# Kernel tuning notes

Measured on AMD Instinct MI355X. Metric: run time of the kernel, lower is better.

## Reference

```python
import jax, jax.numpy as jnp
import numpy as np

NGRAM = 2
NUM_HEADS = 16
NUM_BUCKETS = 32
EMBED_DIM = 1024
REAL_T = 512
BSZ = 4


def setup_inputs() -> dict:
    key = jax.random.key(0)
    ks = jax.random.split(key, 10)
    tgt_len = (1 + NGRAM) * REAL_T
    E, H, NB = EMBED_DIM, NUM_HEADS, NUM_BUCKETS
    w = 0.02
    return {
        "query": jax.random.normal(ks[0], (tgt_len, BSZ, E), jnp.float32),
        "self_attn_mask": jnp.zeros((REAL_T, REAL_T), jnp.float32),
        "ngram_mask_matrix": jnp.zeros((NGRAM, REAL_T, 2 * REAL_T), jnp.float32),
        "i_buckets_main_stream": jax.random.randint(ks[1], (BSZ, REAL_T, REAL_T), 0, NB, jnp.int32),
        "i_bucket_relative_stream": jax.random.randint(ks[2], (BSZ, REAL_T, 2 * REAL_T), 0, NB, jnp.int32),
        "in_proj_weight": jax.random.normal(ks[3], (3 * E, E), jnp.float32) * w,
        "in_proj_bias": jnp.zeros((3 * E,), jnp.float32),
        "out_proj_weight": jax.random.normal(ks[4], (E, E), jnp.float32) * w,
        "out_proj_bias": jnp.zeros((E,), jnp.float32),
        "relative_weight": jax.random.normal(ks[5], (NB * H, E), jnp.float32) * w,
        "relative_bias": jnp.zeros((NB * H,), jnp.float32),
    }


def _forward(query, self_attn_mask, ngram_mask_matrix,
             ib_main, ib_rel,
             in_proj_weight, in_proj_bias, out_proj_weight, out_proj_bias,
             relative_weight, relative_bias):
    tgt_len, bsz, E = query.shape
    H, n = NUM_HEADS, NGRAM
    hd = E // H
    nb = relative_weight.shape[0] // H
    T = tgt_len // (1 + n)
    scaling = hd ** -0.5

    # fused qkv projection
    qkv = query @ in_proj_weight.T + in_proj_bias  # [tgt, B, 3E]
    q, k, v = jnp.split(qkv, 3, axis=-1)
    q = q * scaling

    def to_bh(x):  # [tgt, B, E] -> [B*H, tgt, hd]
        return x.reshape(tgt_len, bsz * H, hd).transpose(1, 0, 2)
    q, k, v = to_bh(q), to_bh(k), to_bh(v)

    h_main = query[:T]                                  # [T, B, E]
    h_pred = query[T:].reshape(n, T, bsz, E)            # [n, T, B, E]
    q_main, k_main, v_main = q[:, :T], k[:, :T], v[:, :T]            # [BH, T, hd]
    def pred(x):  # [BH, n*T, hd] -> [n, BH, T, hd]
        return x[:, T:].reshape(bsz * H, n, T, hd).transpose(1, 0, 2, 3)
    q_pred, k_pred, v_pred = pred(q), pred(k), pred(v)

    # ---- main stream ----
    aw_main = jnp.einsum('bth,bsh->bts', q_main, k_main)  # [BH, T, T]
    # relative bias: per-token bucket values gathered by bucket index
    vals_main = h_main.transpose(1, 0, 2) @ relative_weight.T + relative_bias  # [B, T, nb*H]
    vals_main = vals_main.reshape(bsz, T, nb, H).transpose(0, 3, 1, 2)         # [B, H, T, nb]
    ib = jnp.broadcast_to(ib_main[:, None].astype(jnp.int32), (bsz, H, T, T))
    rel_main = jnp.take_along_axis(vals_main, ib, axis=-1).reshape(bsz * H, T, T)
    aw_main = aw_main + rel_main + self_attn_mask[None]
    p_main = jax.nn.softmax(aw_main, axis=-1)
    attn_main = jnp.einsum('bts,bsh->bth', p_main, v_main)  # [BH, T, hd]
    attn_main = attn_main.transpose(1, 0, 2).reshape(T, bsz, E)

    # ---- ngram predict streams ----
    k_ng = jnp.concatenate([jnp.broadcast_to(k_main[None], (n,) + k_main.shape), k_pred], axis=2)  # [n, BH, 2T, hd]
    v_ng = jnp.concatenate([jnp.broadcast_to(v_main[None], (n,) + v_main.shape), v_pred], axis=2)
    aw_ng = jnp.einsum('nbtc,nbsc->nbts', q_pred, k_ng)  # [n, BH, T, 2T]

    vals_ng = h_pred.transpose(0, 2, 1, 3) @ relative_weight.T + relative_bias  # [n, B, T, nb*H]
    vals_ng = vals_ng.reshape(n, bsz, T, nb, H).transpose(0, 1, 4, 2, 3)        # [n, B, H, T, nb]
    ibr = jnp.broadcast_to(ib_rel[None, :, None].astype(jnp.int32), (n, bsz, H, T, 2 * T))
    rel_ng = jnp.take_along_axis(vals_ng, ibr, axis=-1).reshape(n, bsz * H, T, 2 * T)
    aw_ng = aw_ng + rel_ng + ngram_mask_matrix[:, None]
    p_ng = jax.nn.softmax(aw_ng, axis=-1)
    attn_ng = jnp.einsum('nbts,nbsc->nbtc', p_ng, v_ng)  # [n, BH, T, hd]
    attn_ng = attn_ng.transpose(0, 2, 1, 3).reshape(n * T, bsz, E)

    attn = jnp.concatenate([attn_main, attn_ng], axis=0)  # [tgt, B, E]
    return attn @ out_proj_weight.T + out_proj_bias


def reference(query, self_attn_mask, ngram_mask_matrix,
              i_buckets_main_stream, i_bucket_relative_stream,
              in_proj_weight, in_proj_bias, out_proj_weight, out_proj_bias,
              relative_weight, relative_bias):
    return _forward(query, self_attn_mask, ngram_mask_matrix,
                    i_buckets_main_stream, i_bucket_relative_stream,
                    in_proj_weight, in_proj_bias, out_proj_weight, out_proj_bias,
                    relative_weight, relative_bias)
```

## Files before the change

kernel.cpp:

```cpp
#include <hip/hip_runtime.h>

#define TSEQ 512
#define BSZN 4
#define NH 16
#define NBN 32
#define EMB 1024
#define HD 64
#define TGT 1536
#define MROWS 6144
#define LOG2E 1.44269504088896f

typedef unsigned short ushort_t;
typedef __bf16 bf8 __attribute__((ext_vector_type(8)));
typedef __bf16 bf2_t __attribute__((ext_vector_type(2)));
typedef ushort_t u16x8v __attribute__((ext_vector_type(8)));
typedef float f32x4 __attribute__((ext_vector_type(4)));

__device__ __forceinline__ unsigned short f2bf(float f) {
  return __builtin_bit_cast(unsigned short, (__bf16)f);
}

__device__ __forceinline__ float bf2f(unsigned short u) {
  return __builtin_bit_cast(float, (unsigned int)u << 16);
}

__device__ __forceinline__ unsigned int packbf(float a, float b) {
  bf2_t t;
  t[0] = (__bf16)a;
  t[1] = (__bf16)b;
  return __builtin_bit_cast(unsigned int, t);
}

__device__ __forceinline__ void gload16(const void* g, void* l) {
  __builtin_amdgcn_global_load_lds(
      (const __attribute__((address_space(1))) void*)g,
      (__attribute__((address_space(3))) void*)l, 16, 0, 0);
}

__device__ __forceinline__ f32x4 mfma_bf16(bf8 a, bf8 b, f32x4 c) {
  return __builtin_amdgcn_mfma_f32_16x16x32_bf16(a, b, c, 0, 0, 0);
}

__device__ __forceinline__ float lanebcast(float v, int srclane) {
  return __builtin_bit_cast(float,
      __builtin_amdgcn_ds_bpermute(srclane * 4, __builtin_bit_cast(int, v)));
}

__global__ void prep_all_kernel(const float* __restrict__ q, const float* __restrict__ win,
                                const float* __restrict__ wout, const float* __restrict__ wrel,
                                const int* __restrict__ ibm, const int* __restrict__ ibr,
                                const float* __restrict__ mm, const float* __restrict__ mng,
                                ushort_t* __restrict__ qo, ushort_t* __restrict__ wino,
                                ushort_t* __restrict__ wouto, ushort_t* __restrict__ wrelo,
                                unsigned int* __restrict__ cm, unsigned int* __restrict__ cng) {
  const int i = blockIdx.x * blockDim.x + threadIdx.x;
  const int n0 = 1572864, n1 = 786432, n2 = 262144, n3 = 131072;
  const int ncvt = n0 + n1 + n2 + n3;
  const int nm = 262144, nr = 1048576;
  if (i < ncvt) {
    const float* src;
    ushort_t* dst;
    int off;
    if (i < n0) { src = q; dst = qo; off = i; }
    else if (i < n0 + n1) { src = win; dst = wino; off = i - n0; }
    else if (i < n0 + n1 + n2) { src = wout; dst = wouto; off = i - n0 - n1; }
    else { src = wrel; dst = wrelo; off = i - n0 - n1 - n2; }
    const float4 v = reinterpret_cast<const float4*>(src)[off];
    ushort4 o;
    o.x = f2bf(v.x); o.y = f2bf(v.y); o.z = f2bf(v.z); o.w = f2bf(v.w);
    reinterpret_cast<ushort4*>(dst)[off] = o;
  } else if (i < ncvt + nm) {
    const int f = (i - ncvt) * 4;
    const int4 ib = *reinterpret_cast<const int4*>(ibm + f);
    const float4 mk = *reinterpret_cast<const float4*>(mm + (f & 262143));
    uint4 o;
    o.x = ((unsigned int)f2bf(mk.x * LOG2E) << 16) | ((unsigned int)ib.x & 31u);
    o.y = ((unsigned int)f2bf(mk.y * LOG2E) << 16) | ((unsigned int)ib.y & 31u);
    o.z = ((unsigned int)f2bf(mk.z * LOG2E) << 16) | ((unsigned int)ib.z & 31u);
    o.w = ((unsigned int)f2bf(mk.w * LOG2E) << 16) | ((unsigned int)ib.w & 31u);
    *reinterpret_cast<uint4*>(cm + f) = o;
  } else if (i < ncvt + nm + nr) {
    const int f = (i - ncvt - nm) * 4;
    const int ib_off = ((f >> 20) << 19) + (f & 524287);
    const int mk_off = f & 1048575;
    const int4 ib = *reinterpret_cast<const int4*>(ibr + ib_off);
    const float4 mk = *reinterpret_cast<const float4*>(mng + mk_off);
    uint4 o;
    o.x = ((unsigned int)f2bf(mk.x * LOG2E) << 16) | ((unsigned int)ib.x & 31u);
    o.y = ((unsigned int)f2bf(mk.y * LOG2E) << 16) | ((unsigned int)ib.y & 31u);
    o.z = ((unsigned int)f2bf(mk.z * LOG2E) << 16) | ((unsigned int)ib.z & 31u);
    o.w = ((unsigned int)f2bf(mk.w * LOG2E) << 16) | ((unsigned int)ib.w & 31u);
    *reinterpret_cast<uint4*>(cng + f) = o;
  }
}

template <int MODE>
__global__ __launch_bounds__(256) void gemm_bt(
    const ushort_t* __restrict__ A, const ushort_t* __restrict__ B,
    const float* __restrict__ bias, float* __restrict__ Cf,
    ushort_t* __restrict__ Qo, ushort_t* __restrict__ Ko, ushort_t* __restrict__ Vto,
    int M, int N, int K) {
  __shared__ ushort_t lds[16384];
  ushort_t* lA = lds;
  ushort_t* lB = lds + 8192;

  const int tid = threadIdx.x;
  const int lane = tid & 63;
  const int wid = tid >> 6;
  const int l15 = lane & 15, l4 = lane >> 4;
  const int bm = blockIdx.y, bn = blockIdx.x;
  const int wm = (wid >> 1) * 64, wn = (wid & 1) * 64;

  f32x4 acc[4][4] = {};

  const int r8 = tid >> 3;
  const int c8 = ((tid & 7) ^ (r8 & 7)) * 8;
  const ushort_t* Ag = A + (size_t)(bm * 128 + r8) * K + c8;
  const ushort_t* Bg = B + (size_t)(bn * 128 + r8) * K + c8;
  ushort_t* lAp = lA + tid * 8;
  ushort_t* lBp = lB + tid * 8;

  for (int kt = 0; kt < K; kt += 64) {
    __syncthreads();
#pragma unroll
    for (int i = 0; i < 4; ++i) {
      gload16(Ag + (size_t)i * 32 * K + kt, lAp + i * 2048);
      gload16(Bg + (size_t)i * 32 * K + kt, lBp + i * 2048);
    }
    __syncthreads();
#pragma unroll
    for (int k0 = 0; k0 < 2; ++k0) {
      bf8 af[4], bv[4];
#pragma unroll
      for (int mi = 0; mi < 4; ++mi) {
        const int row = wm + mi * 16 + l15;
        const int slot = (k0 * 4 + l4) ^ (row & 7);
        af[mi] = *reinterpret_cast<const bf8*>(lA + row * 64 + slot * 8);
      }
#pragma unroll
      for (int ni = 0; ni < 4; ++ni) {
        const int row = wn + ni * 16 + l15;
        const int slot = (k0 * 4 + l4) ^ (row & 7);
        bv[ni] = *reinterpret_cast<const bf8*>(lB + row * 64 + slot * 8);
      }
#pragma unroll
      for (int mi = 0; mi < 4; ++mi)
#pragma unroll
        for (int ni = 0; ni < 4; ++ni)
          acc[mi][ni] = mfma_bf16(af[mi], bv[ni], acc[mi][ni]);
    }
  }

  if (MODE == 0 && bn >= 16) {
    __syncthreads();
    char* tb = reinterpret_cast<char*>(lds);
#pragma unroll
    for (int ni = 0; ni < 4; ++ni) {
      const int colloc = wn + ni * 16 + l15;
      const float bc = bias[bn * 128 + colloc];
      const unsigned int swz = (colloc & 7) << 4;
#pragma unroll
      for (int mi = 0; mi < 4; ++mi) {
        const int t_loc = (wm >> 2) + mi * 4 + l4;
        f32x4 v = acc[mi][ni];
#pragma unroll
        for (int r = 0; r < 4; ++r) {
          const int byteoff = colloc * 256 + ((r * 64 + t_loc * 2) ^ swz);
          *reinterpret_cast<ushort_t*>(tb + byteoff) = f2bf(v[r] + bc);
        }
      }
    }
    __syncthreads();
    const int tglob0 = bm * 32;
#pragma unroll
    for (int p = 0; p < 2; ++p) {
      const int pair = wid * 2 + p;
      const int bb = pair >> 1;
      const int hl = pair & 1;
      const int hh = (bn - 16) * 2 + hl;
      const int bh = bb * NH + hh;
      const int tch = lane & 3;
#pragma unroll
      for (int ii = 0; ii < 4; ++ii) {
        const int dloc = ii * 16 + (lane >> 2);
        const int colloc = hl * 64 + dloc;
        const int byteoff = colloc * 256 + ((bb * 64 + tch * 16) ^ ((colloc & 7) << 4));
        const u16x8v val = *reinterpret_cast<const u16x8v*>(tb + byteoff);
        *reinterpret_cast<u16x8v*>(
            Vto + ((size_t)bh * HD + dloc) * TGT + tglob0 + tch * 8) = val;
      }
    }
    return;
  }

#pragma unroll
  for (int ni = 0; ni < 4; ++ni) {
    const int col = bn * 128 + wn + ni * 16 + l15;
    const float bc = bias[col];
#pragma unroll
    for (int mi = 0; mi < 4; ++mi) {
      const int row0 = bm * 128 + wm + mi * 16 + l4 * 4;
      f32x4 v = acc[mi][ni];
#pragma unroll
      for (int r = 0; r < 4; ++r) {
        const int row = row0 + r;
        float val = v[r] + bc;
        if (MODE == 0) {
          const int part = col >> 10;
          const int cc = col & 1023;
          const int h = cc >> 6, d = cc & 63;
          const int t = row >> 2, bb = row & 3;
          const int bh = bb * NH + h;
          if (part == 0) {
            Qo[((size_t)bh * TGT + t) * HD + d] = f2bf(val * (0.125f * LOG2E));
          } else {
            Ko[((size_t)bh * TGT + t) * HD + d] = f2bf(val);
          }
        } else if (MODE == 3) {
          const int hh = col & 15, nb = col >> 4;
          const int qg = row >> 2, bb2 = row & 3;
          Qo[(((size_t)(bb2 * NH + hh)) * TGT + qg) * NBN + nb] = f2bf(val * LOG2E);
        } else {
          Cf[(size_t)row * N + col] = val;
        }
      }
    }
  }
}

__global__ __launch_bounds__(256, 3) void attn_kernel(
    const ushort_t* __restrict__ Q, const ushort_t* __restrict__ Kb,
    const ushort_t* __restrict__ Vt, const ushort_t* __restrict__ VMh,
    const unsigned int* __restrict__ comb_main, const unsigned int* __restrict__ comb_ng,
    ushort_t* __restrict__ AT) {
  __shared__ unsigned char kbuf[2][8192];
  __shared__ unsigned char vbuf[2][8192];
  __shared__ ushort_t vmt16[4][1088];
  __shared__ unsigned int pbl[4][576];

  const int tid = threadIdx.x;
  const int lane = tid & 63, wid = tid >> 6;
  const int l15 = lane & 15, l4 = lane >> 4;

  const int n = blockIdx.x;
  const int xcd = n & 7;
  const int b = xcd >> 1;
  const int idx = (xcd & 1) * 96 + (n >> 3);
  const int h = idx / 12;
  const int rem = idx - h * 12;
  const int z = rem >> 2;
  const int blk = rem & 3;
  const int g = (z == 0) ? 0 : z - 1;
  const int bh = b * NH + h;
  const int t0 = blk * 128 + wid * 32;
  const int qrow0 = (z == 0) ? t0 : TSEQ + g * TSEQ + t0;
  const int nsb = (z == 0) ? 8 : 16;

  {
    const ushort_t* src = VMh + ((size_t)bh * TGT + qrow0) * NBN;
    ushort_t* dst = vmt16[wid];
#pragma unroll
    for (int half = 0; half < 2; ++half) {
      const u16x8v v = *reinterpret_cast<const u16x8v*>(src + half * 512 + lane * 8);
      const int r = half * 16 + (lane >> 2);
      const int c0 = (lane & 3) * 8;
#pragma unroll
      for (int i = 0; i < 8; ++i) dst[r * 34 + c0 + i] = v[i];
    }
  }

  bf8 qf[2][2];
#pragma unroll
  for (int th = 0; th < 2; ++th)
#pragma unroll
    for (int hf = 0; hf < 2; ++hf)
      qf[th][hf] = *reinterpret_cast<const bf8*>(
          &Q[((size_t)bh * TGT + qrow0 + th * 16 + l15) * HD + hf * 32 + l4 * 8]);

  const unsigned int* cb[2];
  {
    const unsigned int* cbase = (z == 0)
        ? comb_main + (size_t)b * TSEQ * TSEQ
        : comb_ng + (size_t)(b * 2 + g) * TSEQ * (2 * TSEQ);
    const int sstr = (z == 0) ? TSEQ : 2 * TSEQ;
    cb[0] = cbase + (size_t)(t0 + l15) * sstr;
    cb[1] = cbase + (size_t)(t0 + 16 + l15) * sstr;
  }

  float m_run[2] = {-1e30f, -1e30f};
  float l_run[2] = {0.f, 0.f};
  f32x4 oacc[2][4] = {};

  const int r8 = lane >> 3;
  const int swzs = ((lane & 7) ^ r8) << 4;
  const int swzr = (l15 & 7) << 4;

  auto stage = [&](int sb, int bf) {
    const int srow0 = (sb < 8) ? sb * 64 : TSEQ + g * TSEQ + (sb - 8) * 64;
    const ushort_t* ks = Kb + ((size_t)bh * TGT + srow0 + wid * 16 + r8) * HD + (swzs >> 1);
    gload16(ks, &kbuf[bf][wid * 2048 + lane * 16]);
    gload16(ks + 8 * HD, &kbuf[bf][wid * 2048 + 1024 + lane * 16]);
    const ushort_t* vs = Vt + ((size_t)bh * HD + wid * 16 + r8) * TGT + srow0 + (swzs >> 1);
    gload16(vs, &vbuf[bf][wid * 2048 + lane * 16]);
    gload16(vs + 8 * TGT, &vbuf[bf][wid * 2048 + 1024 + lane * 16]);
  };

  stage(0, 0);
  asm volatile("s_waitcnt vmcnt(0)" ::: "memory");
  __builtin_amdgcn_s_barrier();

  int cur = 0;
  for (int sb = 0; sb < nsb; ++sb) {
    const int scol = sb * 64;
    if (sb + 1 < nsb) stage(sb + 1, cur ^ 1);

    const unsigned char* kb = kbuf[cur];
    const unsigned char* vbb = vbuf[cur];

    bf8 kf[4][2];
#pragma unroll
    for (int j = 0; j < 4; ++j) {
      const int row = j * 16 + l15;
      kf[j][0] = *reinterpret_cast<const bf8*>(kb + row * 128 + ((l4 * 16) ^ swzr));
      kf[j][1] = *reinterpret_cast<const bf8*>(kb + row * 128 + ((64 + l4 * 16) ^ swzr));
    }

#pragma unroll
    for (int th = 0; th < 2; ++th) {
      const unsigned int* cwp = cb[th] + scol + l4 * 4;
      const uint4 c0 = *reinterpret_cast<const uint4*>(cwp);
      const uint4 c1 = *reinterpret_cast<const uint4*>(cwp + 16);
      const uint4 c2 = *reinterpret_cast<const uint4*>(cwp + 32);
      const uint4 c3 = *reinterpret_cast<const uint4*>(cwp + 48);
      const unsigned int cwa[4][4] = {{c0.x, c0.y, c0.z, c0.w},
                                      {c1.x, c1.y, c1.z, c1.w},
                                      {c2.x, c2.y, c2.z, c2.w},
                                      {c3.x, c3.y, c3.z, c3.w}};
      f32x4 st[4];
#pragma unroll
      for (int j = 0; j < 4; ++j) {
        f32x4 s4 = {};
        s4 = mfma_bf16(kf[j][0], qf[th][0], s4);
        s4 = mfma_bf16(kf[j][1], qf[th][1], s4);
        st[j] = s4;
      }
      const ushort_t* vrow = vmt16[wid] + (th * 16 + l15) * 34;
      float vals[4][4];
      float mx = -1e30f;
#pragma unroll
      for (int j = 0; j < 4; ++j) {
#pragma unroll
        for (int r = 0; r < 4; ++r) {
          const unsigned int w = cwa[j][r];
          const float v = st[j][r] + __builtin_bit_cast(float, w & 0xffff0000u) +
                          bf2f(vrow[w & 31u]);
          vals[j][r] = v;
          mx = fmaxf(mx, v);
        }
      }
      mx = fmaxf(mx, __shfl_xor(mx, 16));
      mx = fmaxf(mx, __shfl_xor(mx, 32));

      const float oldm = m_run[th];
      if (!__all(mx - oldm <= 8.f)) {
        const float newm = fmaxf(oldm, mx);
        const float fct = (oldm <= -1e30f) ? 0.f : exp2f(oldm - newm);
        f32x4 rs;
        rs[0] = lanebcast(fct, l4 * 4 + 0);
        rs[1] = lanebcast(fct, l4 * 4 + 1);
        rs[2] = lanebcast(fct, l4 * 4 + 2);
        rs[3] = lanebcast(fct, l4 * 4 + 3);
#pragma unroll
        for (int dt = 0; dt < 4; ++dt) oacc[th][dt] *= rs;
        l_run[th] *= fct;
        m_run[th] = newm;
      }
      const float mref = m_run[th];

      unsigned int pk[4][2];
      float lsum = 0.f;
#pragma unroll
      for (int j = 0; j < 4; ++j) {
        const float p0 = exp2f(vals[j][0] - mref);
        const float p1 = exp2f(vals[j][1] - mref);
        const float p2 = exp2f(vals[j][2] - mref);
        const float p3 = exp2f(vals[j][3] - mref);
        lsum += (p0 + p1) + (p2 + p3);
        pk[j][0] = packbf(p0, p1);
        pk[j][1] = packbf(p2, p3);
      }
      lsum += __shfl_xor(lsum, 16);
      lsum += __shfl_xor(lsum, 32);
      l_run[th] += lsum;

      {
        unsigned int* prow = &pbl[wid][l15 * 36];
#pragma unroll
        for (int j = 0; j < 4; ++j) {
          uint2 w2;
          w2.x = pk[j][0];
          w2.y = pk[j][1];
          *reinterpret_cast<uint2*>(&prow[j * 8 + l4 * 2]) = w2;
        }
      }
      const unsigned char* pbase = reinterpret_cast<const unsigned char*>(&pbl[wid][0]);
#pragma unroll
      for (int k32 = 0; k32 < 2; ++k32) {
        const bf8 pa = *reinterpret_cast<const bf8*>(
            pbase + l15 * 144 + k32 * 64 + l4 * 16);
#pragma unroll
        for (int dt = 0; dt < 4; ++dt) {
          const bf8 vb = *reinterpret_cast<const bf8*>(
              vbb + (dt * 16 + l15) * 128 + ((k32 * 64 + l4 * 16) ^ swzr));
          oacc[th][dt] = mfma_bf16(pa, vb, oacc[th][dt]);
        }
      }
    }

    asm volatile("s_waitcnt vmcnt(0)" ::: "memory");
    __builtin_amdgcn_s_barrier();
    cur ^= 1;
  }

#pragma unroll
  for (int th = 0; th < 2; ++th) {
    const float linv = 1.f / l_run[th];
    f32x4 bs;
    bs[0] = lanebcast(linv, l4 * 4 + 0);
    bs[1] = lanebcast(linv, l4 * 4 + 1);
    bs[2] = lanebcast(linv, l4 * 4 + 2);
    bs[3] = lanebcast(linv, l4 * 4 + 3);
#pragma unroll
    for (int dt = 0; dt < 4; ++dt) {
#pragma unroll
      for (int r = 0; r < 4; ++r) {
        const int tout = qrow0 + th * 16 + l4 * 4 + r;
        AT[((size_t)tout * BSZN + b) * EMB + h * HD + dt * 16 + l15] =
            f2bf(oacc[th][dt][r] * bs[r]);
      }
    }
  }
}

extern "C" void kernel_launch(void* const* d_in, const int* in_sizes, int n_in,
                              void* d_out, int out_size, void* d_ws, size_t ws_size,
                              hipStream_t stream) {
  const float* query     = (const float*)d_in[0];
  const float* mask_main = (const float*)d_in[1];
  const float* mask_ng   = (const float*)d_in[2];
  const int*   ib_main   = (const int*)d_in[3];
  const int*   ib_rel    = (const int*)d_in[4];
  const float* w_in      = (const float*)d_in[5];
  const float* b_in      = (const float*)d_in[6];
  const float* w_out     = (const float*)d_in[7];
  const float* b_out     = (const float*)d_in[8];
  const float* w_rel     = (const float*)d_in[9];
  const float* b_rel     = (const float*)d_in[10];
  float* out = (float*)d_out;

  ushort_t* qbf    = (ushort_t*)d_ws;
  ushort_t* winbf  = qbf + 6291456;
  ushort_t* woutbf = winbf + 3145728;
  ushort_t* relwbf = woutbf + 1048576;
  ushort_t* Qb     = relwbf + 524288;
  ushort_t* Kbuf   = Qb + 6291456;
  ushort_t* Vtb    = Kbuf + 6291456;
  ushort_t* VMh    = Vtb + 6291456;
  unsigned int* comb_main = (unsigned int*)(VMh + 3145728);
  unsigned int* comb_ng   = comb_main + 1048576;
  ushort_t* AT     = qbf;

  {
    const int total = 2752512 + 262144 + 1048576;
    prep_all_kernel<<<(total + 255) / 256, 256, 0, stream>>>(
        query, w_in, w_out, w_rel, ib_main, ib_rel, mask_main, mask_ng,
        qbf, winbf, woutbf, relwbf, comb_main, comb_ng);
  }

  gemm_bt<0><<<dim3(24, 48), 256, 0, stream>>>(qbf, winbf, b_in, nullptr,
                                               Qb, Kbuf, Vtb, MROWS, 3072, 1024);
  gemm_bt<3><<<dim3(4, 48), 256, 0, stream>>>(qbf, relwbf, b_rel, nullptr,
                                              VMh, nullptr, nullptr, MROWS, 512, 1024);
  attn_kernel<<<768, 256, 0, stream>>>(Qb, Kbuf, Vtb, VMh, comb_main, comb_ng, AT);
  gemm_bt<2><<<dim3(8, 48), 256, 0, stream>>>(AT, woutbf, b_out, out,
                                              nullptr, nullptr, nullptr, MROWS, 1024, 1024);
}
```

Measured before the change: 212.8 us.

## Fuse relative-bucket GEMM into QKV GEMM launch and add MFMA priority hints

Merges the relative-position projection GEMM into the QKV projection launch by adding four extra column-blocks that read the relative weights and write the bucket-value tensor. This removes one kernel launch and its tail, and fills the grid more evenly. It also wraps MFMA sequences in s_setprio in both the GEMM and attention kernels, and hoists the comb-word loads and both S MFMA tiles ahead of the softmax in the attention loop. The hoisting raises register pressure in the attention kernel, which is launched with an occupancy bound of 3.

```diff
diff --git a/kernel.cpp b/kernel.cpp
--- a/kernel.cpp
+++ b/kernel.cpp
@@ -99,7 +99,8 @@
     const ushort_t* __restrict__ A, const ushort_t* __restrict__ B,
     const float* __restrict__ bias, float* __restrict__ Cf,
     ushort_t* __restrict__ Qo, ushort_t* __restrict__ Ko, ushort_t* __restrict__ Vto,
-    int M, int N, int K) {
+    const ushort_t* __restrict__ B2, const float* __restrict__ bias2,
+    ushort_t* __restrict__ VMo, int M, int N, int K) {
   __shared__ ushort_t lds[16384];
   ushort_t* lA = lds;
   ushort_t* lB = lds + 8192;
@@ -110,13 +111,15 @@
   const int l15 = lane & 15, l4 = lane >> 4;
   const int bm = blockIdx.y, bn = blockIdx.x;
   const int wm = (wid >> 1) * 64, wn = (wid & 1) * 64;
+  const bool isrel = (MODE == 0) && (bn >= 24);
 
   f32x4 acc[4][4] = {};
 
   const int r8 = tid >> 3;
   const int c8 = ((tid & 7) ^ (r8 & 7)) * 8;
   const ushort_t* Ag = A + (size_t)(bm * 128 + r8) * K + c8;
-  const ushort_t* Bg = B + (size_t)(bn * 128 + r8) * K + c8;
+  const ushort_t* Bg = isrel ? B2 + (size_t)((bn - 24) * 128 + r8) * K + c8
+                             : B + (size_t)(bn * 128 + r8) * K + c8;
   ushort_t* lAp = lA + tid * 8;
   ushort_t* lBp = lB + tid * 8;
 
@@ -143,15 +146,17 @@
         const int slot = (k0 * 4 + l4) ^ (row & 7);
         bv[ni] = *reinterpret_cast<const bf8*>(lB + row * 64 + slot * 8);
       }
+      __builtin_amdgcn_s_setprio(1);
 #pragma unroll
       for (int mi = 0; mi < 4; ++mi)
 #pragma unroll
         for (int ni = 0; ni < 4; ++ni)
           acc[mi][ni] = mfma_bf16(af[mi], bv[ni], acc[mi][ni]);
-    }
-  }
-
-  if (MODE == 0 && bn >= 16) {
+      __builtin_amdgcn_s_setprio(0);
+    }
+  }
+
+  if (MODE == 0 && bn >= 16 && bn < 24) {
     __syncthreads();
     char* tb = reinterpret_cast<char*>(lds);
 #pragma unroll
@@ -195,8 +200,10 @@
 
 #pragma unroll
   for (int ni = 0; ni < 4; ++ni) {
-    const int col = bn * 128 + wn + ni * 16 + l15;
-    const float bc = bias[col];
+    const int colloc = wn + ni * 16 + l15;
+    const int col = bn * 128 + colloc;
+    const int colrel = (bn - 24) * 128 + colloc;
+    const float bc = isrel ? bias2[colrel] : bias[col];
 #pragma unroll
     for (int mi = 0; mi < 4; ++mi) {
       const int row0 = bm * 128 + wm + mi * 16 + l4 * 4;
@@ -206,20 +213,21 @@
         const int row = row0 + r;
         float val = v[r] + bc;
         if (MODE == 0) {
-          const int part = col >> 10;
-          const int cc = col & 1023;
-          const int h = cc >> 6, d = cc & 63;
-          const int t = row >> 2, bb = row & 3;
-          const int bh = bb * NH + h;
-          if (part == 0) {
-            Qo[((size_t)bh * TGT + t) * HD + d] = f2bf(val * (0.125f * LOG2E));
+          if (isrel) {
+            const int hh = colrel & 15, nb = colrel >> 4;
+            const int qg = row >> 2, bb2 = row & 3;
+            VMo[(((size_t)(bb2 * NH + hh)) * TGT + qg) * NBN + nb] = f2bf(val * LOG2E);
           } else {
-            Ko[((size_t)bh * TGT + t) * HD + d] = f2bf(val);
+            const int cc = col & 1023;
+            const int h = cc >> 6, d = cc & 63;
+            const int t = row >> 2, bb = row & 3;
+            const int bh = bb * NH + h;
+            if (col < 1024) {
+              Qo[((size_t)bh * TGT + t) * HD + d] = f2bf(val * (0.125f * LOG2E));
+            } else {
+              Ko[((size_t)bh * TGT + t) * HD + d] = f2bf(val);
+            }
           }
-        } else if (MODE == 3) {
-          const int hh = col & 15, nb = col >> 4;
-          const int qg = row >> 2, bb2 = row & 3;
-          Qo[(((size_t)(bb2 * NH + hh)) * TGT + qg) * NBN + nb] = f2bf(val * LOG2E);
         } else {
           Cf[(size_t)row * N + col] = val;
         }
@@ -317,6 +325,16 @@
     const unsigned char* kb = kbuf[cur];
     const unsigned char* vbb = vbuf[cur];
 
+    uint4 cw[2][4];
+#pragma unroll
+    for (int th = 0; th < 2; ++th) {
+      const unsigned int* cwp = cb[th] + scol + l4 * 4;
+      cw[th][0] = *reinterpret_cast<const uint4*>(cwp);
+      cw[th][1] = *reinterpret_cast<const uint4*>(cwp + 16);
+      cw[th][2] = *reinterpret_cast<const uint4*>(cwp + 32);
+      cw[th][3] = *reinterpret_cast<const uint4*>(cwp + 48);
+    }
+
     bf8 kf[4][2];
 #pragma unroll
     for (int j = 0; j < 4; ++j) {
@@ -324,39 +342,33 @@
       kf[j][0] = *reinterpret_cast<const bf8*>(kb + row * 128 + ((l4 * 16) ^ swzr));
       kf[j][1] = *reinterpret_cast<const bf8*>(kb + row * 128 + ((64 + l4 * 16) ^ swzr));
     }
-
-#pragma unroll
-    for (int th = 0; th < 2; ++th) {
-      const unsigned int* cwp = cb[th] + scol + l4 * 4;
-      const uint4 c0 = *reinterpret_cast<const uint4*>(cwp);
-      const uint4 c1 = *reinterpret_cast<const uint4*>(cwp + 16);
-      const uint4 c2 = *reinterpret_cast<const uint4*>(cwp + 32);
-      const uint4 c3 = *reinterpret_cast<const uint4*>(cwp + 48);
-      const unsigned int cwa[4][4] = {{c0.x, c0.y, c0.z, c0.w},
-                                      {c1.x, c1.y, c1.z, c1.w},
-                                      {c2.x, c2.y, c2.z, c2.w},
-                                      {c3.x, c3.y, c3.z, c3.w}};
-      f32x4 st[4];
+    f32x4 st[2][4];
+    __builtin_amdgcn_s_setprio(1);
+#pragma unroll
+    for (int th = 0; th < 2; ++th)
 #pragma unroll
       for (int j = 0; j < 4; ++j) {
         f32x4 s4 = {};
         s4 = mfma_bf16(kf[j][0], qf[th][0], s4);
         s4 = mfma_bf16(kf[j][1], qf[th][1], s4);
-        st[j] = s4;
-      }
+        st[th][j] = s4;
+      }
+    __builtin_amdgcn_s_setprio(0);
+
+#pragma unroll
+    for (int th = 0; th < 2; ++th) {
       const ushort_t* vrow = vmt16[wid] + (th * 16 + l15) * 34;
       float vals[4][4];
       float mx = -1e30f;
 #pragma unroll
       for (int j = 0; j < 4; ++j) {
-#pragma unroll
-        for (int r = 0; r < 4; ++r) {
-          const unsigned int w = cwa[j][r];
-          const float v = st[j][r] + __builtin_bit_cast(float, w & 0xffff0000u) +
-                          bf2f(vrow[w & 31u]);
-          vals[j][r] = v;
-          mx = fmaxf(mx, v);
-        }
+        const unsigned int w0 = cw[th][j].x, w1 = cw[th][j].y;
+        const unsigned int w2 = cw[th][j].z, w3 = cw[th][j].w;
+        vals[j][0] = st[th][j][0] + __builtin_bit_cast(float, w0 & 0xffff0000u) + bf2f(vrow[w0 & 31u]);
+        vals[j][1] = st[th][j][1] + __builtin_bit_cast(float, w1 & 0xffff0000u) + bf2f(vrow[w1 & 31u]);
+        vals[j][2] = st[th][j][2] + __builtin_bit_cast(float, w2 & 0xffff0000u) + bf2f(vrow[w2 & 31u]);
+        vals[j][3] = st[th][j][3] + __builtin_bit_cast(float, w3 & 0xffff0000u) + bf2f(vrow[w3 & 31u]);
+        mx = fmaxf(mx, fmaxf(fmaxf(vals[j][0], vals[j][1]), fmaxf(vals[j][2], vals[j][3])));
       }
       mx = fmaxf(mx, __shfl_xor(mx, 16));
       mx = fmaxf(mx, __shfl_xor(mx, 32));
@@ -397,10 +409,10 @@
         unsigned int* prow = &pbl[wid][l15 * 36];
 #pragma unroll
         for (int j = 0; j < 4; ++j) {
-          uint2 w2;
-          w2.x = pk[j][0];
-          w2.y = pk[j][1];
-          *reinterpret_cast<uint2*>(&prow[j * 8 + l4 * 2]) = w2;
+          uint2 w2v;
+          w2v.x = pk[j][0];
+          w2v.y = pk[j][1];
+          *reinterpret_cast<uint2*>(&prow[j * 8 + l4 * 2]) = w2v;
         }
       }
       const unsigned char* pbase = reinterpret_cast<const unsigned char*>(&pbl[wid][0]);
@@ -408,12 +420,14 @@
       for (int k32 = 0; k32 < 2; ++k32) {
         const bf8 pa = *reinterpret_cast<const bf8*>(
             pbase + l15 * 144 + k32 * 64 + l4 * 16);
+        __builtin_amdgcn_s_setprio(1);
 #pragma unroll
         for (int dt = 0; dt < 4; ++dt) {
           const bf8 vb = *reinterpret_cast<const bf8*>(
               vbb + (dt * 16 + l15) * 128 + ((k32 * 64 + l4 * 16) ^ swzr));
           oacc[th][dt] = mfma_bf16(pa, vb, oacc[th][dt]);
         }
+        __builtin_amdgcn_s_setprio(0);
       }
     }
 
@@ -477,11 +491,11 @@
         qbf, winbf, woutbf, relwbf, comb_main, comb_ng);
   }
 
-  gemm_bt<0><<<dim3(24, 48), 256, 0, stream>>>(qbf, winbf, b_in, nullptr,
-                                               Qb, Kbuf, Vtb, MROWS, 3072, 1024);
-  gemm_bt<3><<<dim3(4, 48), 256, 0, stream>>>(qbf, relwbf, b_rel, nullptr,
-                                              VMh, nullptr, nullptr, MROWS, 512, 1024);
+  gemm_bt<0><<<dim3(28, 48), 256, 0, stream>>>(qbf, winbf, b_in, nullptr,
+                                               Qb, Kbuf, Vtb, relwbf, b_rel, VMh,
+                                               MROWS, 3072, 1024);
   attn_kernel<<<768, 256, 0, stream>>>(Qb, Kbuf, Vtb, VMh, comb_main, comb_ng, AT);
   gemm_bt<2><<<dim3(8, 48), 256, 0, stream>>>(AT, woutbf, b_out, out,
-                                              nullptr, nullptr, nullptr, MROWS, 1024, 1024);
-}
+                                              nullptr, nullptr, nullptr, nullptr, nullptr,
+                                              nullptr, MROWS, 1024, 1024);
+}
```

Result: faster. 194.2 us (-8.7%).
